# Kernel optimization log

Measured on AMD Instinct MI355X. Metric: run time of the kernel, lower is better.

The kernel has to match this reference:

```python
import jax, jax.numpy as jnp
import numpy as np

D = 512       # d_model
H = 8         # n_heads
L = 6         # n_blocks
DFF = 2048    # d_ffn
IN_DIM = 4096
OUT_DIM = 1000
B = 8
S = 512
DK = D // H
EPS = 1e-5
NEG = -1e9    # masked_fill value from source (-1000000000.0)

# sinusoidal positional encoding table (matches Positional_Encoding)
_pos = np.arange(5000)[:, None].astype(np.float64)
_div = np.exp(np.arange(0, D, 2) * (-np.log(10000.0) / D))
_pe = np.zeros((5000, D), np.float32)
_pe[:, 0::2] = np.sin(_pos * _div)
_pe[:, 1::2] = np.cos(_pos * _div)
PE = jnp.asarray(_pe)


def _ln(x, g, b):
    m = jnp.mean(x, -1, keepdims=True)
    v = jnp.var(x, -1, keepdims=True)
    return (x - m) * jax.lax.rsqrt(v + EPS) * g + b


def _attn(q, k, v, causal):
    # q:[B,Sq,D], k/v:[B,Sk,D] -> multi-head attention with source's quirky mask
    b, sq, _ = q.shape
    sk = k.shape[1]
    q = q.reshape(b, sq, H, DK).transpose(0, 2, 1, 3)
    k = k.reshape(b, sk, H, DK).transpose(0, 2, 1, 3)
    v = v.reshape(b, sk, H, DK).transpose(0, 2, 1, 3)
    s = jnp.einsum('bhqd,bhkd->bhqk', q, k) / jnp.sqrt(jnp.asarray(DK, q.dtype))
    mask = s != 0.0  # faithful: source masks positions where score == padding (0)
    if causal:
        mask = mask & jnp.tril(jnp.ones((sq, sk), bool))
    s = jnp.where(mask, s, NEG)
    p = jax.nn.softmax(s, axis=-1)
    o = jnp.einsum('bhqk,bhkd->bhqd', p, v)
    return o.transpose(0, 2, 1, 3).reshape(b, sq, D)


def _ffn(x, w1, b1, w2, b2):
    return jax.nn.relu(x @ w1 + b1) @ w2 + b2


def setup_inputs() -> dict:
    key = jax.random.key(0)
    ks = iter(jax.random.split(key, 40))

    def w(shape, s=0.02):
        return jax.random.normal(next(ks), shape, jnp.float32) * s

    inp = {}
    inp['x'] = jax.random.randint(next(ks), (B, S), 0, IN_DIM)
    inp['target'] = jax.random.randint(next(ks), (B,), 0, OUT_DIM)
    inp['in_emb'] = w((IN_DIM, D), 1.0)
    inp['out_emb'] = w((OUT_DIM, D), 1.0)
    # encoder params (stacked over layers)
    inp['enc_qkv_w'] = w((L, 3, D, D))
    inp['enc_qkv_b'] = w((L, 3, D))
    inp['enc_ln1_g'] = jnp.ones((L, D), jnp.float32)
    inp['enc_ln1_b'] = jnp.zeros((L, D), jnp.float32)
    inp['enc_ffn1_w'] = w((L, D, DFF))
    inp['enc_ffn1_b'] = w((L, DFF))
    inp['enc_ffn2_w'] = w((L, DFF, D))
    inp['enc_ffn2_b'] = w((L, D))
    inp['enc_ln2_g'] = jnp.ones((L, D), jnp.float32)
    inp['enc_ln2_b'] = jnp.zeros((L, D), jnp.float32)
    # decoder params
    inp['dec_qkv1_w'] = w((L, 3, D, D))
    inp['dec_qkv1_b'] = w((L, 3, D))
    inp['dec_ln1_g'] = jnp.ones((L, D), jnp.float32)
    inp['dec_ln1_b'] = jnp.zeros((L, D), jnp.float32)
    inp['dec_qkv2_w'] = w((L, 3, D, D))
    inp['dec_qkv2_b'] = w((L, 3, D))
    inp['dec_ln2_g'] = jnp.ones((L, D), jnp.float32)
    inp['dec_ln2_b'] = jnp.zeros((L, D), jnp.float32)
    inp['dec_ffn1_w'] = w((L, D, DFF))
    inp['dec_ffn1_b'] = w((L, DFF))
    inp['dec_ffn2_w'] = w((L, DFF, D))
    inp['dec_ffn2_b'] = w((L, D))
    inp['dec_ln3_g'] = jnp.ones((L, D), jnp.float32)
    inp['dec_ln3_b'] = jnp.zeros((L, D), jnp.float32)
    inp['out_w'] = w((D, OUT_DIM))
    inp['out_b'] = w((OUT_DIM,))
    return inp


def reference(x, target, in_emb, out_emb,
              enc_qkv_w, enc_qkv_b, enc_ln1_g, enc_ln1_b,
              enc_ffn1_w, enc_ffn1_b, enc_ffn2_w, enc_ffn2_b,
              enc_ln2_g, enc_ln2_b,
              dec_qkv1_w, dec_qkv1_b, dec_ln1_g, dec_ln1_b,
              dec_qkv2_w, dec_qkv2_b, dec_ln2_g, dec_ln2_b,
              dec_ffn1_w, dec_ffn1_b, dec_ffn2_w, dec_ffn2_b,
              dec_ln3_g, dec_ln3_b, out_w, out_b):
    scale = jnp.sqrt(jnp.float32(D))
    # encoder: embed tokens + positional encoding (dropout is identity at eval)
    e = in_emb[x] * scale + PE[None, :S]
    for i in range(L):
        q = e @ enc_qkv_w[i, 0] + enc_qkv_b[i, 0]
        k = e @ enc_qkv_w[i, 1] + enc_qkv_b[i, 1]
        v = e @ enc_qkv_w[i, 2] + enc_qkv_b[i, 2]
        e = _ln(_attn(q, k, v, False) + e, enc_ln1_g[i], enc_ln1_b[i])
        e = _ln(e + _ffn(e, enc_ffn1_w[i], enc_ffn1_b[i], enc_ffn2_w[i], enc_ffn2_b[i]),
                enc_ln2_g[i], enc_ln2_b[i])
    # decoder: target.unsqueeze(1) -> seq len 1
    d = out_emb[target][:, None, :] * scale + PE[None, :1]
    for i in range(L):
        q = d @ dec_qkv1_w[i, 0] + dec_qkv1_b[i, 0]
        k = d @ dec_qkv1_w[i, 1] + dec_qkv1_b[i, 1]
        v = d @ dec_qkv1_w[i, 2] + dec_qkv1_b[i, 2]
        d = _ln(_attn(q, k, v, True) + d, dec_ln1_g[i], dec_ln1_b[i])
        q = d @ dec_qkv2_w[i, 0] + dec_qkv2_b[i, 0]
        k = e @ dec_qkv2_w[i, 1] + dec_qkv2_b[i, 1]
        v = e @ dec_qkv2_w[i, 2] + dec_qkv2_b[i, 2]
        d = _ln(_attn(q, k, v, False) + d, dec_ln2_g[i], dec_ln2_b[i])
        d = _ln(d + _ffn(d, dec_ffn1_w[i], dec_ffn1_b[i], dec_ffn2_w[i], dec_ffn2_b[i]),
                dec_ln3_g[i], dec_ln3_b[i])
    return d @ out_w + out_b  # [B, 1, OUT_DIM] logits (source never applies its softmax)
```

## Files before the change

kernel.cpp:

```cpp
#include <hip/hip_runtime.h>
#include <hip/hip_bf16.h>

#define DM 512
#define NH 8
#define DK 64
#define SEQ 512
#define NB 8
#define NL 6
#define DFF 2048
#define OUTD 1000
#define EMB_SCALE 22.627416997969522f
#define PE_C (-0.017988946039015984f)

typedef __bf16 bf16x8 __attribute__((ext_vector_type(8)));
typedef __bf16 bf16x4 __attribute__((ext_vector_type(4)));
typedef float f32x4 __attribute__((ext_vector_type(4)));

__device__ __forceinline__ void load16_lds(const __bf16* g, __bf16* l) {
  __builtin_amdgcn_global_load_lds(
      (const __attribute__((address_space(1))) void*)g,
      (__attribute__((address_space(3))) void*)l, 16, 0, 0);
}

__device__ __forceinline__ float dot8(bf16x8 w, const float* a) {
  float s = 0.f;
#pragma unroll
  for (int j = 0; j < 8; ++j) s += (float)w[j] * a[j];
  return s;
}

__global__ __launch_bounds__(256) void pe_kernel(float* __restrict__ pe) {
  int s = blockIdx.x;
  int d2 = threadIdx.x;
  float div = expf((float)(2 * d2) * PE_C);
  float arg = (float)s * div;
  pe[(size_t)s * DM + 2 * d2] = sinf(arg);
  pe[(size_t)s * DM + 2 * d2 + 1] = cosf(arg);
}

__global__ __launch_bounds__(256) void embed_enc(const int* __restrict__ x,
                                                 const float* __restrict__ emb,
                                                 const float* __restrict__ pe,
                                                 float* __restrict__ e,
                                                 __bf16* __restrict__ eb) {
  int idx = blockIdx.x * 256 + threadIdx.x;
  int d = idx & (DM - 1);
  int bs = idx >> 9;
  int s = bs & (SEQ - 1);
  int tok = x[bs];
  float v = emb[(size_t)tok * DM + d] * EMB_SCALE + pe[(size_t)s * DM + d];
  e[idx] = v;
  eb[idx] = (__bf16)v;
}

__global__ __launch_bounds__(256) void embed_dec(const int* __restrict__ t,
                                                 const float* __restrict__ emb,
                                                 float* __restrict__ dd) {
  int idx = blockIdx.x * 256 + threadIdx.x;
  int d = idx & (DM - 1);
  int b = idx >> 9;
  float pe = (d & 1) ? 1.0f : 0.0f;
  dd[idx] = emb[(size_t)t[b] * DM + d] * EMB_SCALE + pe;
}

__global__ __launch_bounds__(256) void transpose_w(const float* __restrict__ W,
                                                   __bf16* __restrict__ WT,
                                                   int K, int N) {
  __shared__ float t[32][33];
  size_t off = (size_t)blockIdx.z * K * N;
  W += off; WT += off;
  int k0 = blockIdx.y * 32, n0 = blockIdx.x * 32;
  int tx = threadIdx.x & 7, ty = threadIdx.x >> 3;
  float4 v = *(const float4*)&W[(size_t)(k0 + ty) * N + n0 + tx * 4];
  t[ty][tx * 4 + 0] = v.x; t[ty][tx * 4 + 1] = v.y;
  t[ty][tx * 4 + 2] = v.z; t[ty][tx * 4 + 3] = v.w;
  __syncthreads();
  bf16x4 o;
  o[0] = (__bf16)t[tx * 4 + 0][ty];
  o[1] = (__bf16)t[tx * 4 + 1][ty];
  o[2] = (__bf16)t[tx * 4 + 2][ty];
  o[3] = (__bf16)t[tx * 4 + 3][ty];
  *(bf16x4*)&WT[(size_t)(n0 + ty) * K + k0 + tx * 4] = o;
}

__global__ __launch_bounds__(256) void transpose_ow(const float* __restrict__ W,
                                                    __bf16* __restrict__ WT) {
  __shared__ float t[32][33];
  int n0 = blockIdx.x * 32, k0 = blockIdx.y * 32;
  int tid = threadIdx.x;
  for (int i = tid; i < 1024; i += 256) {
    int kk = i >> 5, nn = i & 31;
    t[kk][nn] = (n0 + nn < OUTD) ? W[(size_t)(k0 + kk) * OUTD + n0 + nn] : 0.f;
  }
  __syncthreads();
  for (int i = tid; i < 1024; i += 256) {
    int nn = i >> 5, kk = i & 31;
    if (n0 + nn < OUTD)
      WT[(size_t)(n0 + nn) * DM + k0 + kk] = (__bf16)t[kk][nn];
  }
}

template <int BN, bool RELU, bool WF32, bool WBF16, bool TRV, bool KVM>
__global__ __launch_bounds__(256) void mfma_gemm(
    const __bf16* __restrict__ A, const __bf16* __restrict__ BT,
    const float* __restrict__ bias, float* __restrict__ C,
    __bf16* __restrict__ Cb, __bf16* __restrict__ Vt, int M, int N, int K,
    long btStride, long bStride, long cStride) {
  int z = blockIdx.z;
  if (KVM) {
    long idx = (long)(z >> 1) * 3 + 1 + (z & 1);
    BT += idx * btStride;
    bias += idx * bStride;
  } else {
    BT += (size_t)z * btStride;
    bias += (size_t)z * bStride;
  }
  if (WF32) C += (size_t)z * cStride;
  if (WBF16) Cb += (size_t)z * cStride;

  constexpr int NI = BN / 32;
  __shared__ __bf16 As[2][128 * 64];
  __shared__ __bf16 Bs[2][BN * 64];

  int tid = threadIdx.x;
  int wave = tid >> 6, lane = tid & 63;
  int wm = wave >> 1, wn = wave & 1;
  int quad = lane >> 4, l16 = lane & 15;
  int rlane = lane >> 3, c8 = lane & 7;
  int m0 = blockIdx.y * 128, n0 = blockIdx.x * BN;
  int gcol = ((c8 ^ rlane) * 8);

  f32x4 acc[4][NI];
#pragma unroll
  for (int i = 0; i < 4; ++i)
#pragma unroll
    for (int j = 0; j < NI; ++j) acc[i][j] = (f32x4){0.f, 0.f, 0.f, 0.f};

  auto stage = [&](int buf, int k0) {
#pragma unroll
    for (int j = 0; j < 4; ++j) {
      int row = j * 32 + wave * 8 + rlane;
      load16_lds(&A[(size_t)(m0 + row) * K + k0 + gcol],
                 &As[buf][(j * 32 + wave * 8) * 64]);
    }
#pragma unroll
    for (int j = 0; j < BN / 32; ++j) {
      int row = j * 32 + wave * 8 + rlane;
      load16_lds(&BT[(size_t)(n0 + row) * K + k0 + gcol],
                 &Bs[buf][(j * 32 + wave * 8) * 64]);
    }
  };

  const int NT = K >> 6;
  stage(0, 0);
  __syncthreads();
  for (int t = 0; t < NT; ++t) {
    int cur = t & 1;
    if (t + 1 < NT) stage(cur ^ 1, (t + 1) << 6);
#pragma unroll
    for (int kk = 0; kk < 64; kk += 32) {
      bf16x8 af[4], bf[NI];
#pragma unroll
      for (int i = 0; i < 4; ++i) {
        int row = wm * 64 + i * 16 + l16;
        af[i] = *(const bf16x8*)&As[cur][row * 64 + ((((kk >> 3) + quad) ^ (row & 7)) * 8)];
      }
#pragma unroll
      for (int i = 0; i < NI; ++i) {
        int row = wn * (BN / 2) + i * 16 + l16;
        bf[i] = *(const bf16x8*)&Bs[cur][row * 64 + ((((kk >> 3) + quad) ^ (row & 7)) * 8)];
      }
#pragma unroll
      for (int mi = 0; mi < 4; ++mi)
#pragma unroll
        for (int ni = 0; ni < NI; ++ni)
          acc[mi][ni] = __builtin_amdgcn_mfma_f32_16x16x32_bf16(
              af[mi], bf[ni], acc[mi][ni], 0, 0, 0);
    }
    __syncthreads();
  }

#pragma unroll
  for (int ni = 0; ni < NI; ++ni) {
    int col = n0 + wn * (BN / 2) + ni * 16 + l16;
    float bv = bias[col];
    if (TRV && z == 2) {
      int b = m0 >> 9;
#pragma unroll
      for (int mi = 0; mi < 4; ++mi) {
        int srow = (m0 & 511) + wm * 64 + mi * 16 + quad * 4;
        bf16x4 pk;
#pragma unroll
        for (int r = 0; r < 4; ++r) pk[r] = (__bf16)(acc[mi][ni][r] + bv);
        *(bf16x4*)&Vt[((size_t)(b * 512 + col)) * 512 + srow] = pk;
      }
    } else {
#pragma unroll
      for (int mi = 0; mi < 4; ++mi) {
#pragma unroll
        for (int r = 0; r < 4; ++r) {
          int row = m0 + wm * 64 + mi * 16 + quad * 4 + r;
          float v = acc[mi][ni][r] + bv;
          if (RELU) v = fmaxf(v, 0.f);
          if (WF32) C[(size_t)row * N + col] = v;
          if (WBF16) Cb[(size_t)row * N + col] = (__bf16)v;
        }
      }
    }
  }
}

#define SCP 520
__global__ __launch_bounds__(256) void attn_mfma(const __bf16* __restrict__ QKV,
                                                 const __bf16* __restrict__ Vt,
                                                 float* __restrict__ O) {
  __shared__ __bf16 Sc[16 * SCP];
  __shared__ __bf16 Tt[2][64 * 64];

  const long ACTL = (long)NB * SEQ * DM;
  int tid = threadIdx.x;
  int wave = tid >> 6, lane = tid & 63;
  int quad = lane >> 4, l16 = lane & 15;
  int rlane = lane >> 3, c8 = lane & 7;
  int q0 = blockIdx.x * 16;
  int bh = blockIdx.y, b = bh >> 3, h = bh & 7;
  const __bf16* Q = QKV;
  const __bf16* Kp = QKV + ACTL;
  size_t baseQ = ((size_t)b * SEQ + q0) * DM + h * DK;
  size_t baseK = ((size_t)b * SEQ) * DM + h * DK;
  const __bf16* VtB = Vt + ((size_t)(b * 512 + h * 64)) * 512;
  int gcol = (c8 ^ rlane) * 8;

  bf16x8 af0 = *(const bf16x8*)&Q[baseQ + (size_t)l16 * DM + quad * 8];
  bf16x8 af1 = *(const bf16x8*)&Q[baseQ + (size_t)l16 * DM + 32 + quad * 8];

  auto stageK = [&](int buf, int kt) {
#pragma unroll
    for (int j = 0; j < 2; ++j) {
      int row = j * 32 + wave * 8 + rlane;
      load16_lds(&Kp[baseK + (size_t)(kt * 64 + row) * DM + gcol],
                 &Tt[buf][(j * 32 + wave * 8) * 64]);
    }
  };
  auto stageV = [&](int buf, int kt) {
#pragma unroll
    for (int j = 0; j < 2; ++j) {
      int row = j * 32 + wave * 8 + rlane;
      load16_lds(&VtB[(size_t)row * 512 + kt * 64 + gcol],
                 &Tt[buf][(j * 32 + wave * 8) * 64]);
    }
  };

  stageK(0, 0);
  __syncthreads();
  for (int kt = 0; kt < 8; ++kt) {
    int cur = kt & 1;
    if (kt < 7) stageK(cur ^ 1, kt + 1);
    f32x4 acc = (f32x4){0.f, 0.f, 0.f, 0.f};
    int krow = wave * 16 + l16, sw = krow & 7;
    bf16x8 b0 = *(const bf16x8*)&Tt[cur][krow * 64 + ((quad ^ sw) * 8)];
    bf16x8 b1 = *(const bf16x8*)&Tt[cur][krow * 64 + (((4 + quad) ^ sw) * 8)];
    acc = __builtin_amdgcn_mfma_f32_16x16x32_bf16(af0, b0, acc, 0, 0, 0);
    acc = __builtin_amdgcn_mfma_f32_16x16x32_bf16(af1, b1, acc, 0, 0, 0);
#pragma unroll
    for (int r = 0; r < 4; ++r)
      Sc[(quad * 4 + r) * SCP + kt * 64 + wave * 16 + l16] =
          (__bf16)(acc[r] * 0.125f);
    __syncthreads();
  }

  stageV(0, 0);

#pragma unroll
  for (int rr = 0; rr < 4; ++rr) {
    int r = wave * 4 + rr;
    float v[8];
    float mx = -1e30f;
#pragma unroll
    for (int j = 0; j < 8; ++j) {
      v[j] = (float)Sc[r * SCP + j * 64 + lane];
      mx = fmaxf(mx, v[j]);
    }
    for (int o = 32; o > 0; o >>= 1) mx = fmaxf(mx, __shfl_xor(mx, o));
    float sum = 0.f;
#pragma unroll
    for (int j = 0; j < 8; ++j) { v[j] = __expf(v[j] - mx); sum += v[j]; }
    for (int o = 32; o > 0; o >>= 1) sum += __shfl_xor(sum, o);
    float inv = 1.f / sum;
#pragma unroll
    for (int j = 0; j < 8; ++j)
      Sc[r * SCP + j * 64 + lane] = (__bf16)(v[j] * inv);
  }
  __syncthreads();

  f32x4 oacc = (f32x4){0.f, 0.f, 0.f, 0.f};
  for (int kt = 0; kt < 8; ++kt) {
    int cur = kt & 1;
    if (kt < 7) stageV(cur ^ 1, kt + 1);
    int drow = wave * 16 + l16, sw = drow & 7;
#pragma unroll
    for (int kk = 0; kk < 64; kk += 32) {
      bf16x8 pa = *(const bf16x8*)&Sc[l16 * SCP + kt * 64 + kk + quad * 8];
      bf16x8 vb = *(const bf16x8*)&Tt[cur][drow * 64 + ((((kk >> 3) + quad) ^ sw) * 8)];
      oacc = __builtin_amdgcn_mfma_f32_16x16x32_bf16(pa, vb, oacc, 0, 0, 0);
    }
    __syncthreads();
  }
#pragma unroll
  for (int r = 0; r < 4; ++r)
    O[((size_t)b * SEQ + q0 + quad * 4 + r) * DM + h * DK + wave * 16 + l16] =
        oacc[r];
}

template <bool WB>
__global__ __launch_bounds__(256) void add_ln(
    const float* __restrict__ x, const float* __restrict__ res,
    const float* __restrict__ cbias,
    const float* __restrict__ g, const float* __restrict__ beta,
    float* __restrict__ y, __bf16* __restrict__ yb) {
  int row = blockIdx.x;
  int tid = threadIdx.x;
  const float* xr = x + (size_t)row * DM;
  const float* rr = res + (size_t)row * DM;
  float b0 = cbias ? cbias[tid] : 0.f;
  float b1 = cbias ? cbias[tid + 256] : 0.f;
  float v0 = xr[tid] + b0 + rr[tid];
  float v1 = xr[tid + 256] + b1 + rr[tid + 256];
  float s = v0 + v1, sq = v0 * v0 + v1 * v1;
  for (int o = 32; o > 0; o >>= 1) {
    s += __shfl_xor(s, o);
    sq += __shfl_xor(sq, o);
  }
  __shared__ float ps[4], pq[4];
  int wv = tid >> 6;
  if ((tid & 63) == 0) { ps[wv] = s; pq[wv] = sq; }
  __syncthreads();
  s = ps[0] + ps[1] + ps[2] + ps[3];
  sq = pq[0] + pq[1] + pq[2] + pq[3];
  float mean = s * (1.f / DM);
  float var = sq * (1.f / DM) - mean * mean;
  float rstd = rsqrtf(var + 1e-5f);
  float o0 = (v0 - mean) * rstd * g[tid] + beta[tid];
  float o1 = (v1 - mean) * rstd * g[tid + 256] + beta[tid + 256];
  y[(size_t)row * DM + tid] = o0;
  y[(size_t)row * DM + tid + 256] = o1;
  if (WB) {
    yb[(size_t)row * DM + tid] = (__bf16)o0;
    yb[(size_t)row * DM + tid + 256] = (__bf16)o1;
  }
}


__global__ __launch_bounds__(256) void dec_vln(
    float* __restrict__ dd, const __bf16* __restrict__ WvT,
    const float* __restrict__ bv, const float* __restrict__ g,
    const float* __restrict__ beta) {
  __shared__ float arow[DM];
  int r = blockIdx.x, tid = threadIdx.x;
  arow[tid] = dd[(size_t)r * DM + tid];
  arow[tid + 256] = dd[(size_t)r * DM + tid + 256];
  __syncthreads();
  float out[2];
#pragma unroll
  for (int cc = 0; cc < 2; ++cc) {
    int c = tid + cc * 256;
    const __bf16* w = &WvT[(size_t)c * DM];
    float acc = 0.f;
#pragma unroll 4
    for (int k = 0; k < DM; k += 8) acc += dot8(*(const bf16x8*)&w[k], &arow[k]);
    out[cc] = arow[c] + acc + bv[c];
  }
  float s = out[0] + out[1], sq = out[0] * out[0] + out[1] * out[1];
  for (int o = 32; o > 0; o >>= 1) { s += __shfl_xor(s, o); sq += __shfl_xor(sq, o); }
  __shared__ float ps[4], pq[4];
  int wv = tid >> 6;
  if ((tid & 63) == 0) { ps[wv] = s; pq[wv] = sq; }
  __syncthreads();
  s = ps[0] + ps[1] + ps[2] + ps[3];
  sq = pq[0] + pq[1] + pq[2] + pq[3];
  float mean = s * (1.f / DM);
  float rstd = rsqrtf(sq * (1.f / DM) - mean * mean + 1e-5f);
  dd[(size_t)r * DM + tid] = (out[0] - mean) * rstd * g[tid] + beta[tid];
  dd[(size_t)r * DM + tid + 256] = (out[1] - mean) * rstd * g[tid + 256] + beta[tid + 256];
}

__global__ __launch_bounds__(256) void dec_qattn(
    const float* __restrict__ dd, const __bf16* __restrict__ WqT,
    const float* __restrict__ qb, const __bf16* __restrict__ Kb,
    const __bf16* __restrict__ Vb, float* __restrict__ da) {
  __shared__ float arow[DM];
  __shared__ float red[4][64];
  __shared__ float q[64];
  __shared__ float sc[SEQ];
  __shared__ float wred[4];

  int bh = blockIdx.x, b = bh >> 3, h = bh & 7;
  int tid = threadIdx.x, lane = tid & 63, wave = tid >> 6;
  arow[tid] = dd[(size_t)b * DM + tid];
  arow[tid + 256] = dd[(size_t)b * DM + tid + 256];
  __syncthreads();

  {
    int c = tid & 63, s = tid >> 6;
    const __bf16* w = &WqT[(size_t)(h * 64 + c) * DM + s * 128];
    float acc = 0.f;
#pragma unroll
    for (int k = 0; k < 128; k += 8) acc += dot8(*(const bf16x8*)&w[k], &arow[s * 128 + k]);
    red[s][c] = acc;
  }
  __syncthreads();
  if (tid < 64) q[tid] = red[0][tid] + red[1][tid] + red[2][tid] + red[3][tid] + qb[h * 64 + tid];
  __syncthreads();

  for (int key = tid; key < SEQ; key += 256) {
    const __bf16* kp = &Kb[((size_t)b * SEQ + key) * DM + h * 64];
    float acc = 0.f;
#pragma unroll
    for (int k = 0; k < 64; k += 8) acc += dot8(*(const bf16x8*)&kp[k], &q[k]);
    sc[key] = acc * 0.125f;
  }
  __syncthreads();
  float m = -1e30f;
  for (int j = tid; j < SEQ; j += 256) m = fmaxf(m, sc[j]);
  for (int o = 32; o > 0; o >>= 1) m = fmaxf(m, __shfl_xor(m, o));
  if (lane == 0) wred[wave] = m;
  __syncthreads();
  m = fmaxf(fmaxf(wred[0], wred[1]), fmaxf(wred[2], wred[3]));
  float sum = 0.f;
  for (int j = tid; j < SEQ; j += 256) {
    float p = __expf(sc[j] - m);
    sc[j] = p;
    sum += p;
  }
  for (int o = 32; o > 0; o >>= 1) sum += __shfl_xor(sum, o);
  __syncthreads();
  if (lane == 0) wred[wave] = sum;
  __syncthreads();
  float inv = 1.f / (wred[0] + wred[1] + wred[2] + wred[3]);

  {
    int d = tid & 63, s = tid >> 6;
    float acc = 0.f;
    const __bf16* vp = &Vb[((size_t)b * SEQ + s * 128) * DM + h * 64 + d];
#pragma unroll 8
    for (int k = 0; k < 128; ++k) acc += sc[s * 128 + k] * (float)vp[(size_t)k * DM];
    red[s][d] = acc;
  }
  __syncthreads();
  if (tid < 64)
    da[(size_t)b * DM + h * 64 + tid] =
        (red[0][tid] + red[1][tid] + red[2][tid] + red[3][tid]) * inv;
}

__global__ __launch_bounds__(256) void dec_ffn1(
    const float* __restrict__ dd, const __bf16* __restrict__ W1T,
    const float* __restrict__ b1, float* __restrict__ h) {
  __shared__ float a[8][DM];
  int tid = threadIdx.x, lane = tid & 63, wave = tid >> 6;
  for (int i = tid; i < 8 * DM; i += 256) a[i >> 9][i & 511] = dd[i];
  __syncthreads();
  int col = blockIdx.x * 4 + wave;
  bf16x8 w = *(const bf16x8*)&W1T[(size_t)col * DM + lane * 8];
  float acc[8];
#pragma unroll
  for (int r = 0; r < 8; ++r) acc[r] = dot8(w, &a[r][lane * 8]);
#pragma unroll
  for (int r = 0; r < 8; ++r)
    for (int o = 32; o > 0; o >>= 1) acc[r] += __shfl_xor(acc[r], o);
  if (lane == 0) {
    float bb = b1[col];
#pragma unroll
    for (int r = 0; r < 8; ++r) h[(size_t)r * DFF + col] = fmaxf(acc[r] + bb, 0.f);
  }
}

__global__ __launch_bounds__(256) void dec_ffn2(
    const float* __restrict__ h, const __bf16* __restrict__ W2T,
    const float* __restrict__ b2, float* __restrict__ df) {
  __shared__ float red[4][8];
  int tid = threadIdx.x, lane = tid & 63, wave = tid >> 6;
  int c = wave >> 1, half = wave & 1;
  int col = blockIdx.x * 2 + c;
  int k0 = half * 1024 + lane * 8;
  bf16x8 w0 = *(const bf16x8*)&W2T[(size_t)col * DFF + k0];
  bf16x8 w1 = *(const bf16x8*)&W2T[(size_t)col * DFF + k0 + 512];
  float acc[8];
#pragma unroll
  for (int r = 0; r < 8; ++r) {
    float4 h0a = *(const float4*)&h[(size_t)r * DFF + k0];
    float4 h0b = *(const float4*)&h[(size_t)r * DFF + k0 + 4];
    float4 h1a = *(const float4*)&h[(size_t)r * DFF + k0 + 512];
    float4 h1b = *(const float4*)&h[(size_t)r * DFF + k0 + 516];
    float hh0[8] = {h0a.x, h0a.y, h0a.z, h0a.w, h0b.x, h0b.y, h0b.z, h0b.w};
    float hh1[8] = {h1a.x, h1a.y, h1a.z, h1a.w, h1b.x, h1b.y, h1b.z, h1b.w};
    acc[r] = dot8(w0, hh0) + dot8(w1, hh1);
  }
#pragma unroll
  for (int r = 0; r < 8; ++r)
    for (int o = 32; o > 0; o >>= 1) acc[r] += __shfl_xor(acc[r], o);
  if (lane == 0) {
#pragma unroll
    for (int r = 0; r < 8; ++r) red[wave][r] = acc[r];
  }
  __syncthreads();
  if (tid < 16) {
    int cc = tid >> 3, r = tid & 7;
    int ocol = blockIdx.x * 2 + cc;
    df[(size_t)r * DM + ocol] =
        red[cc * 2][r] + red[cc * 2 + 1][r] + b2[ocol];
  }
}

__global__ __launch_bounds__(256) void dec_out(
    const float* __restrict__ dd, const __bf16* __restrict__ WoT,
    const float* __restrict__ ob, float* __restrict__ out) {
  __shared__ float a[8][DM];
  int tid = threadIdx.x, lane = tid & 63, wave = tid >> 6;
  for (int i = tid; i < 8 * DM; i += 256) a[i >> 9][i & 511] = dd[i];
  __syncthreads();
  int col = blockIdx.x * 4 + wave;
  bf16x8 w = *(const bf16x8*)&WoT[(size_t)col * DM + lane * 8];
  float acc[8];
#pragma unroll
  for (int r = 0; r < 8; ++r) acc[r] = dot8(w, &a[r][lane * 8]);
#pragma unroll
  for (int r = 0; r < 8; ++r)
    for (int o = 32; o > 0; o >>= 1) acc[r] += __shfl_xor(acc[r], o);
  if (lane == 0) {
    float bb = ob[col];
#pragma unroll
    for (int r = 0; r < 8; ++r) out[(size_t)r * OUTD + col] = acc[r] + bb;
  }
}

extern "C" void kernel_launch(void* const* d_in, const int* in_sizes, int n_in,
                              void* d_out, int out_size, void* d_ws, size_t ws_size,
                              hipStream_t stream) {
  const int* x = (const int*)d_in[0];
  const int* target = (const int*)d_in[1];
  const float* in_emb = (const float*)d_in[2];
  const float* out_emb = (const float*)d_in[3];
  const float* enc_qkv_w = (const float*)d_in[4];
  const float* enc_qkv_b = (const float*)d_in[5];
  const float* enc_ln1_g = (const float*)d_in[6];
  const float* enc_ln1_b = (const float*)d_in[7];
  const float* enc_ffn1_w = (const float*)d_in[8];
  const float* enc_ffn1_b = (const float*)d_in[9];
  const float* enc_ffn2_w = (const float*)d_in[10];
  const float* enc_ffn2_b = (const float*)d_in[11];
  const float* enc_ln2_g = (const float*)d_in[12];
  const float* enc_ln2_b = (const float*)d_in[13];
  const float* dec_qkv1_w = (const float*)d_in[14];
  const float* dec_qkv1_b = (const float*)d_in[15];
  const float* dec_ln1_g = (const float*)d_in[16];
  const float* dec_ln1_b = (const float*)d_in[17];
  const float* dec_qkv2_w = (const float*)d_in[18];
  const float* dec_qkv2_b = (const float*)d_in[19];
  const float* dec_ln2_g = (const float*)d_in[20];
  const float* dec_ln2_b = (const float*)d_in[21];
  const float* dec_ffn1_w = (const float*)d_in[22];
  const float* dec_ffn1_b = (const float*)d_in[23];
  const float* dec_ffn2_w = (const float*)d_in[24];
  const float* dec_ffn2_b = (const float*)d_in[25];
  const float* dec_ln3_g = (const float*)d_in[26];
  const float* dec_ln3_b = (const float*)d_in[27];
  const float* out_w = (const float*)d_in[28];
  const float* out_b = (const float*)d_in[29];

  const long ACTL = (long)NB * SEQ * DM;
  const int M = NB * SEQ;
  const long WQS = (long)DM * DM;
  const long WFS = (long)DM * DFF;

  char* p = (char*)d_ws;
  float* e = (float*)p;            p += ACTL * 4;
  float* tb = (float*)p;           p += ACTL * 4;
  float* pe = (float*)p;           p += (long)SEQ * DM * 4;
  float* dd = (float*)p;           p += NB * DM * 4;
  float* da = (float*)p;           p += NB * DM * 4;
  float* dh = (float*)p;           p += NB * DFF * 4;
  float* df = (float*)p;           p += NB * DM * 4;
  p = (char*)(((uintptr_t)p + 255) & ~(uintptr_t)255);
  __bf16* eb = (__bf16*)p;         p += ACTL * 2;
  __bf16* qkvb = (__bf16*)p;       p += 3 * ACTL * 2;
  __bf16* hbb = (__bf16*)p;        p += (long)M * DFF * 2;
  __bf16* kvb = (__bf16*)p;        p += 12L * ACTL * 2;
  __bf16* wtq = (__bf16*)p;        p += 18L * WQS * 2;
  __bf16* wtf1 = (__bf16*)p;       p += 6L * WFS * 2;
  __bf16* wtf2 = (__bf16*)p;       p += 6L * WFS * 2;
  __bf16* wtd = (__bf16*)p;        p += 18L * WQS * 2;
  __bf16* wtd1 = (__bf16*)p;       p += 18L * WQS * 2;
  __bf16* wf1t = (__bf16*)p;       p += 6L * WFS * 2;
  __bf16* wf2t = (__bf16*)p;       p += 6L * WFS * 2;
  __bf16* wot = (__bf16*)p;        p += (long)OUTD * DM * 2;

  __bf16* vtb = qkvb + 2 * ACTL;

  pe_kernel<<<SEQ, 256, 0, stream>>>(pe);
  transpose_w<<<dim3(16, 16, 18), 256, 0, stream>>>(enc_qkv_w, wtq, DM, DM);
  transpose_w<<<dim3(64, 16, 6), 256, 0, stream>>>(enc_ffn1_w, wtf1, DM, DFF);
  transpose_w<<<dim3(16, 64, 6), 256, 0, stream>>>(enc_ffn2_w, wtf2, DFF, DM);
  transpose_w<<<dim3(16, 16, 18), 256, 0, stream>>>(dec_qkv2_w, wtd, DM, DM);
  transpose_w<<<dim3(16, 16, 18), 256, 0, stream>>>(dec_qkv1_w, wtd1, DM, DM);
  transpose_w<<<dim3(64, 16, 6), 256, 0, stream>>>(dec_ffn1_w, wf1t, DM, DFF);
  transpose_w<<<dim3(16, 64, 6), 256, 0, stream>>>(dec_ffn2_w, wf2t, DFF, DM);
  transpose_ow<<<dim3(32, 16), 256, 0, stream>>>(out_w, wot);

  embed_enc<<<(M * DM) / 256, 256, 0, stream>>>(x, in_emb, pe, e, eb);
  for (int i = 0; i < NL; ++i) {
    mfma_gemm<128, false, false, true, true, false><<<dim3(4, 32, 3), 256, 0, stream>>>(
        eb, wtq + (size_t)i * 3 * WQS, enc_qkv_b + (size_t)i * 3 * DM,
        nullptr, qkvb, vtb, M, DM, DM, WQS, DM, ACTL);
    attn_mfma<<<dim3(SEQ / 16, NB * NH), 256, 0, stream>>>(qkvb, vtb, tb);
    add_ln<true><<<M, 256, 0, stream>>>(tb, e, nullptr, enc_ln1_g + i * DM,
                                        enc_ln1_b + i * DM, e, eb);
    mfma_gemm<128, true, false, true, false, false><<<dim3(16, 32, 1), 256, 0, stream>>>(
        eb, wtf1 + (size_t)i * WFS, enc_ffn1_b + (size_t)i * DFF,
        nullptr, hbb, nullptr, M, DFF, DM, 0, 0, 0);
    mfma_gemm<64, false, true, false, false, false><<<dim3(8, 32, 1), 256, 0, stream>>>(
        hbb, wtf2 + (size_t)i * WFS, enc_ffn2_b + (size_t)i * DM,
        tb, nullptr, nullptr, M, DM, DFF, 0, 0, 0);
    add_ln<true><<<M, 256, 0, stream>>>(tb, e, nullptr, enc_ln2_g + i * DM,
                                        enc_ln2_b + i * DM, e, eb);
  }

  mfma_gemm<128, false, false, true, false, true><<<dim3(4, 32, 12), 256, 0, stream>>>(
      eb, wtd, dec_qkv2_b, nullptr, kvb, nullptr, M, DM, DM, WQS, DM, ACTL);

  embed_dec<<<(NB * DM) / 256, 256, 0, stream>>>(target, out_emb, dd);
  for (int i = 0; i < NL; ++i) {
    dec_vln<<<8, 256, 0, stream>>>(
        dd, wtd1 + ((size_t)i * 3 + 2) * WQS, dec_qkv1_b + ((size_t)i * 3 + 2) * DM,
        dec_ln1_g + i * DM, dec_ln1_b + i * DM);
    dec_qattn<<<64, 256, 0, stream>>>(
        dd, wtd + (size_t)i * 3 * WQS, dec_qkv2_b + (size_t)i * 3 * DM,
        kvb + (size_t)i * 2 * ACTL, kvb + ((size_t)i * 2 + 1) * ACTL, da);
    add_ln<false><<<NB, 256, 0, stream>>>(
        da, dd, nullptr, dec_ln2_g + i * DM, dec_ln2_b + i * DM, dd, nullptr);
    dec_ffn1<<<DFF / 4, 256, 0, stream>>>(
        dd, wf1t + (size_t)i * WFS, dec_ffn1_b + (size_t)i * DFF, dh);
    dec_ffn2<<<DM / 2, 256, 0, stream>>>(
        dh, wf2t + (size_t)i * WFS, dec_ffn2_b + (size_t)i * DM, df);
    add_ln<false><<<NB, 256, 0, stream>>>(
        df, dd, nullptr, dec_ln3_g + i * DM, dec_ln3_b + i * DM, dd, nullptr);
  }

  dec_out<<<OUTD / 4, 256, 0, stream>>>(dd, wot, out_b, (float*)d_out);
}
```

Baseline: 1.225 ms.

## Use 8-wave GEMM blocks and XCD-aware block remapping for GEMM and attention

The GEMM kernel moves from 4 to 8 waves per block. Each wave now owns a 32-row slice instead of 64 rows, which halves the accumulators per thread, and staging loads are spread across all 8 waves. Both the GEMM and attention kernels remap the linear block index so that blocks sharing the same rows or batch-head land on the same XCD, aiming for better L2 reuse. The risks are more waves competing for LDS and synchronisation per block, and fewer MFMAs per wave to hide latency.

```diff
diff --git a/kernel.cpp b/kernel.cpp
--- a/kernel.cpp
+++ b/kernel.cpp
@@ -101,12 +101,20 @@
 }
 
 template <int BN, bool RELU, bool WF32, bool WBF16, bool TRV, bool KVM>
-__global__ __launch_bounds__(256) void mfma_gemm(
+__global__ __launch_bounds__(512) void mfma_gemm(
     const __bf16* __restrict__ A, const __bf16* __restrict__ BT,
     const float* __restrict__ bias, float* __restrict__ C,
     __bf16* __restrict__ Cb, __bf16* __restrict__ Vt, int M, int N, int K,
     long btStride, long bStride, long cStride) {
-  int z = blockIdx.z;
+  int gx = gridDim.x, gy = gridDim.y;
+  int lin = blockIdx.x + gx * (blockIdx.y + gy * blockIdx.z);
+  int xcd = lin & 7, li = lin >> 3;
+  int yc = gy >> 3;
+  int bx = li % gx;
+  int t2 = li / gx;
+  int by = xcd * yc + (t2 % yc);
+  int z = t2 / yc;
+
   if (KVM) {
     long idx = (long)(z >> 1) * 3 + 1 + (z & 1);
     BT += idx * btStride;
@@ -127,27 +135,27 @@
   int wm = wave >> 1, wn = wave & 1;
   int quad = lane >> 4, l16 = lane & 15;
   int rlane = lane >> 3, c8 = lane & 7;
-  int m0 = blockIdx.y * 128, n0 = blockIdx.x * BN;
+  int m0 = by * 128, n0 = bx * BN;
   int gcol = ((c8 ^ rlane) * 8);
 
-  f32x4 acc[4][NI];
-#pragma unroll
-  for (int i = 0; i < 4; ++i)
+  f32x4 acc[2][NI];
+#pragma unroll
+  for (int i = 0; i < 2; ++i)
 #pragma unroll
     for (int j = 0; j < NI; ++j) acc[i][j] = (f32x4){0.f, 0.f, 0.f, 0.f};
 
   auto stage = [&](int buf, int k0) {
 #pragma unroll
-    for (int j = 0; j < 4; ++j) {
-      int row = j * 32 + wave * 8 + rlane;
-      load16_lds(&A[(size_t)(m0 + row) * K + k0 + gcol],
-                 &As[buf][(j * 32 + wave * 8) * 64]);
-    }
-#pragma unroll
-    for (int j = 0; j < BN / 32; ++j) {
-      int row = j * 32 + wave * 8 + rlane;
-      load16_lds(&BT[(size_t)(n0 + row) * K + k0 + gcol],
-                 &Bs[buf][(j * 32 + wave * 8) * 64]);
+    for (int j = 0; j < 2; ++j) {
+      int rb = j * 64 + wave * 8;
+      load16_lds(&A[(size_t)(m0 + rb + rlane) * K + k0 + gcol],
+                 &As[buf][rb * 64]);
+    }
+#pragma unroll
+    for (int j = 0; j < BN / 64; ++j) {
+      int rb = j * 64 + wave * 8;
+      load16_lds(&BT[(size_t)(n0 + rb + rlane) * K + k0 + gcol],
+                 &Bs[buf][rb * 64]);
     }
   };
 
@@ -159,23 +167,23 @@
     if (t + 1 < NT) stage(cur ^ 1, (t + 1) << 6);
 #pragma unroll
     for (int kk = 0; kk < 64; kk += 32) {
-      bf16x8 af[4], bf[NI];
-#pragma unroll
-      for (int i = 0; i < 4; ++i) {
-        int row = wm * 64 + i * 16 + l16;
+      bf16x8 af[2], bfr[NI];
+#pragma unroll
+      for (int i = 0; i < 2; ++i) {
+        int row = wm * 32 + i * 16 + l16;
         af[i] = *(const bf16x8*)&As[cur][row * 64 + ((((kk >> 3) + quad) ^ (row & 7)) * 8)];
       }
 #pragma unroll
       for (int i = 0; i < NI; ++i) {
         int row = wn * (BN / 2) + i * 16 + l16;
-        bf[i] = *(const bf16x8*)&Bs[cur][row * 64 + ((((kk >> 3) + quad) ^ (row & 7)) * 8)];
+        bfr[i] = *(const bf16x8*)&Bs[cur][row * 64 + ((((kk >> 3) + quad) ^ (row & 7)) * 8)];
       }
 #pragma unroll
-      for (int mi = 0; mi < 4; ++mi)
+      for (int mi = 0; mi < 2; ++mi)
 #pragma unroll
         for (int ni = 0; ni < NI; ++ni)
           acc[mi][ni] = __builtin_amdgcn_mfma_f32_16x16x32_bf16(
-              af[mi], bf[ni], acc[mi][ni], 0, 0, 0);
+              af[mi], bfr[ni], acc[mi][ni], 0, 0, 0);
     }
     __syncthreads();
   }
@@ -187,8 +195,8 @@
     if (TRV && z == 2) {
       int b = m0 >> 9;
 #pragma unroll
-      for (int mi = 0; mi < 4; ++mi) {
-        int srow = (m0 & 511) + wm * 64 + mi * 16 + quad * 4;
+      for (int mi = 0; mi < 2; ++mi) {
+        int srow = (m0 & 511) + wm * 32 + mi * 16 + quad * 4;
         bf16x4 pk;
 #pragma unroll
         for (int r = 0; r < 4; ++r) pk[r] = (__bf16)(acc[mi][ni][r] + bv);
@@ -196,10 +204,10 @@
       }
     } else {
 #pragma unroll
-      for (int mi = 0; mi < 4; ++mi) {
+      for (int mi = 0; mi < 2; ++mi) {
 #pragma unroll
         for (int r = 0; r < 4; ++r) {
-          int row = m0 + wm * 64 + mi * 16 + quad * 4 + r;
+          int row = m0 + wm * 32 + mi * 16 + quad * 4 + r;
           float v = acc[mi][ni][r] + bv;
           if (RELU) v = fmaxf(v, 0.f);
           if (WF32) C[(size_t)row * N + col] = v;
@@ -222,8 +230,12 @@
   int wave = tid >> 6, lane = tid & 63;
   int quad = lane >> 4, l16 = lane & 15;
   int rlane = lane >> 3, c8 = lane & 7;
-  int q0 = blockIdx.x * 16;
-  int bh = blockIdx.y, b = bh >> 3, h = bh & 7;
+  int lin = blockIdx.x + gridDim.x * blockIdx.y;
+  int xcd = lin & 7, li = lin >> 3;
+  int yc = gridDim.y >> 3;
+  int q0 = (li % gridDim.x) * 16;
+  int bh = xcd * yc + li / gridDim.x;
+  int b = bh >> 3, h = bh & 7;
   const __bf16* Q = QKV;
   const __bf16* Kp = QKV + ACTL;
   size_t baseQ = ((size_t)b * SEQ + q0) * DM + h * DK;
@@ -608,23 +620,23 @@
 
   embed_enc<<<(M * DM) / 256, 256, 0, stream>>>(x, in_emb, pe, e, eb);
   for (int i = 0; i < NL; ++i) {
-    mfma_gemm<128, false, false, true, true, false><<<dim3(4, 32, 3), 256, 0, stream>>>(
+    mfma_gemm<128, false, false, true, true, false><<<dim3(4, 32, 3), 512, 0, stream>>>(
         eb, wtq + (size_t)i * 3 * WQS, enc_qkv_b + (size_t)i * 3 * DM,
         nullptr, qkvb, vtb, M, DM, DM, WQS, DM, ACTL);
     attn_mfma<<<dim3(SEQ / 16, NB * NH), 256, 0, stream>>>(qkvb, vtb, tb);
     add_ln<true><<<M, 256, 0, stream>>>(tb, e, nullptr, enc_ln1_g + i * DM,
                                         enc_ln1_b + i * DM, e, eb);
-    mfma_gemm<128, true, false, true, false, false><<<dim3(16, 32, 1), 256, 0, stream>>>(
+    mfma_gemm<128, true, false, true, false, false><<<dim3(16, 32, 1), 512, 0, stream>>>(
         eb, wtf1 + (size_t)i * WFS, enc_ffn1_b + (size_t)i * DFF,
         nullptr, hbb, nullptr, M, DFF, DM, 0, 0, 0);
-    mfma_gemm<64, false, true, false, false, false><<<dim3(8, 32, 1), 256, 0, stream>>>(
+    mfma_gemm<64, false, true, false, false, false><<<dim3(8, 32, 1), 512, 0, stream>>>(
         hbb, wtf2 + (size_t)i * WFS, enc_ffn2_b + (size_t)i * DM,
         tb, nullptr, nullptr, M, DM, DFF, 0, 0, 0);
     add_ln<true><<<M, 256, 0, stream>>>(tb, e, nullptr, enc_ln2_g + i * DM,
                                         enc_ln2_b + i * DM, e, eb);
   }
 
-  mfma_gemm<128, false, false, true, false, true><<<dim3(4, 32, 12), 256, 0, stream>>>(
+  mfma_gemm<128, false, false, true, false, true><<<dim3(4, 32, 12), 512, 0, stream>>>(
       eb, wtd, dec_qkv2_b, nullptr, kvb, nullptr, M, DM, DM, WQS, DM, ACTL);
 
   embed_dec<<<(NB * DM) / 256, 256, 0, stream>>>(target, out_emb, dd);
```

Result: faster. 1.157 ms (-5.5%).
